# Optimization experiments

Measured on AMD Instinct MI355X. Metric: run time of the kernel, lower is better.

The kernel has to match this reference:

```python
import jax, jax.numpy as jnp
import numpy as np

D_IN = 1024
D_OUT = 1024

def setup_inputs() -> dict:
    key = jax.random.key(0)
    ks = jax.random.split(key, 7)
    s = 1.0 / np.sqrt(D_IN)
    x = jax.random.normal(ks[0], (4, 2048, D_IN), dtype=jnp.float32)
    Wq = jax.random.uniform(ks[1], (D_IN, D_OUT), jnp.float32, -s, s)
    Wk = jax.random.uniform(ks[2], (D_IN, D_OUT), jnp.float32, -s, s)
    Wv = jax.random.uniform(ks[3], (D_IN, D_OUT), jnp.float32, -s, s)
    bq = jax.random.uniform(ks[4], (D_OUT,), jnp.float32, -s, s)
    bk = jax.random.uniform(ks[5], (D_OUT,), jnp.float32, -s, s)
    bv = jax.random.uniform(ks[6], (D_OUT,), jnp.float32, -s, s)
    return {"x": x, "Wq": Wq, "Wk": Wk, "Wv": Wv, "bq": bq, "bk": bk, "bv": bv}

def reference(x, Wq, Wk, Wv, bq, bk, bv):
    # x: [b, n, d_in]
    q = jnp.einsum('bnd,de->bne', x, Wq) + bq
    k = jnp.einsum('bnd,de->bne', x, Wk) + bk
    v = jnp.einsum('bnd,de->bne', x, Wv) + bv
    scale = 1.0 / jnp.sqrt(jnp.asarray(k.shape[-1], dtype=x.dtype))
    scores = jnp.einsum('bqe,bke->bqk', q, k) * scale  # [b, n, n]
    weights = jax.nn.softmax(scores, axis=-1)
    return jnp.einsum('bqk,bke->bqe', weights, v)
```

## Files before the change

kernel.cpp:

```cpp
#include <hip/hip_runtime.h>
#include <cstdint>

typedef __bf16 bf16x8 __attribute__((ext_vector_type(8)));
typedef float f32x16 __attribute__((ext_vector_type(16)));
typedef float f32x4 __attribute__((ext_vector_type(4)));

__device__ __forceinline__ unsigned short f2b(float f) {
    union { float f; uint32_t u; } x; x.f = f;
    uint32_t r = (x.u + 0x7fffu + ((x.u >> 16) & 1u)) >> 16;
    return (unsigned short)r;
}
__device__ __forceinline__ float b2f(unsigned short h) {
    union { float f; uint32_t u; } x; x.u = ((uint32_t)h) << 16;
    return x.f;
}

__global__ __launch_bounds__(256) void convert_x_kernel(const float* __restrict__ x,
                                                        unsigned short* __restrict__ xb) {
    int i = (blockIdx.x * 256 + threadIdx.x) * 4;
    float4 v = *(const float4*)(x + i);
    ushort4 o;
    o.x = f2b(v.x); o.y = f2b(v.y); o.z = f2b(v.z); o.w = f2b(v.w);
    *(ushort4*)(xb + i) = o;
}

__global__ __launch_bounds__(1024) void transpose_w_kernel(const float* __restrict__ Wq,
                                                           const float* __restrict__ Wk,
                                                           const float* __restrict__ Wv,
                                                           unsigned short* __restrict__ Wt) {
    __shared__ float tile[32][33];
    const float* W = (blockIdx.z == 0) ? Wq : (blockIdx.z == 1) ? Wk : Wv;
    int n0 = blockIdx.x * 32, k0 = blockIdx.y * 32;
    int tx = threadIdx.x, ty = threadIdx.y;
    tile[ty][tx] = W[(k0 + ty) * 1024 + n0 + tx];
    __syncthreads();
    Wt[((long)blockIdx.z * 1024 + n0 + ty) * 1024 + k0 + tx] = f2b(tile[tx][ty]);
}

template <int EPI>
__global__ __launch_bounds__(256) void gemm32(const unsigned short* __restrict__ A, int lda, long sA,
                                              const unsigned short* __restrict__ Bm, int ldb, long sB,
                                              void* __restrict__ Cv, long sC, int K,
                                              const float* __restrict__ bq, const float* __restrict__ bk,
                                              const float* __restrict__ bv,
                                              unsigned short* __restrict__ Qb,
                                              unsigned short* __restrict__ Kb,
                                              unsigned short* __restrict__ Vt) {
    __shared__ unsigned short As0[128 * 64];
    __shared__ unsigned short Bs0[128 * 64];
    __shared__ unsigned short As1[128 * 64];
    __shared__ unsigned short Bs1[128 * 64];

    const int tid = threadIdx.x;
    const int wave = tid >> 6, lane = tid & 63;
    const int h = lane >> 5;
    const int l31 = lane & 31;
    const int wm = wave >> 1, wn = wave & 1;
    const long bm = (long)blockIdx.y * 128;
    const long bn = (long)blockIdx.x * 128;

    const unsigned short* Ab = A + (long)blockIdx.z * sA;
    const unsigned short* Bb = Bm + (long)blockIdx.z * sB;

    f32x16 acc[2][2];
#pragma unroll
    for (int mi = 0; mi < 2; ++mi) {
#pragma unroll
        for (int ni = 0; ni < 2; ++ni) {
#pragma unroll
            for (int r = 0; r < 16; ++r) acc[mi][ni][r] = 0.0f;
        }
    }

    const int srow_in = lane >> 3;
    const int cswz = (lane & 7) ^ srow_in;
    const unsigned short* aptr[4];
    const unsigned short* bptr[4];
    int sloff[4];
#pragma unroll
    for (int j = 0; j < 4; ++j) {
        const int row = j * 32 + wave * 8 + srow_in;
        aptr[j] = Ab + (bm + row) * (long)lda + cswz * 8;
        bptr[j] = Bb + (bn + row) * (long)ldb + cswz * 8;
        sloff[j] = (j * 32 + wave * 8) * 64;
    }

    const int arow0 = (wm * 64 + l31) * 64;
    const int brow0 = (wn * 64 + l31) * 64;
    int sw[4];
#pragma unroll
    for (int kh = 0; kh < 4; ++kh)
        sw[kh] = (((2 * kh + h) ^ (lane & 7)) * 8);

#define STAGE(AsB, BsB, kofs)                                                                           \
    do {                                                                                                \
        _Pragma("unroll")                                                                               \
        for (int j = 0; j < 4; ++j) {                                                                   \
            __builtin_amdgcn_global_load_lds(                                                           \
                (const __attribute__((address_space(1))) void*)(aptr[j] + (kofs)),                      \
                (__attribute__((address_space(3))) void*)(&AsB[sloff[j]]), 16, 0, 0);                   \
            __builtin_amdgcn_global_load_lds(                                                           \
                (const __attribute__((address_space(1))) void*)(bptr[j] + (kofs)),                      \
                (__attribute__((address_space(3))) void*)(&BsB[sloff[j]]), 16, 0, 0);                   \
        }                                                                                               \
    } while (0)

#define COMPUTE_T(AsB, BsB)                                                                             \
    do {                                                                                                \
        _Pragma("unroll")                                                                               \
        for (int kp = 0; kp < 2; ++kp) {                                                                \
            bf16x8 af[2][2], bfr[2][2];                                                                 \
            _Pragma("unroll")                                                                           \
            for (int mi = 0; mi < 2; ++mi) {                                                            \
                _Pragma("unroll")                                                                       \
                for (int kk = 0; kk < 2; ++kk) {                                                        \
                    af[mi][kk] = *(const bf16x8*)&AsB[arow0 + mi * 32 * 64 + sw[kp * 2 + kk]];          \
                }                                                                                       \
            }                                                                                           \
            _Pragma("unroll")                                                                           \
            for (int ni = 0; ni < 2; ++ni) {                                                            \
                _Pragma("unroll")                                                                       \
                for (int kk = 0; kk < 2; ++kk) {                                                        \
                    bfr[ni][kk] = *(const bf16x8*)&BsB[brow0 + ni * 32 * 64 + sw[kp * 2 + kk]];         \
                }                                                                                       \
            }                                                                                           \
            _Pragma("unroll")                                                                           \
            for (int kk = 0; kk < 2; ++kk) {                                                            \
                _Pragma("unroll")                                                                       \
                for (int mi = 0; mi < 2; ++mi) {                                                        \
                    _Pragma("unroll")                                                                   \
                    for (int ni = 0; ni < 2; ++ni) {                                                    \
                        acc[mi][ni] = __builtin_amdgcn_mfma_f32_32x32x16_bf16(af[mi][kk], bfr[ni][kk],  \
                                                                              acc[mi][ni], 0, 0, 0);    \
                    }                                                                                   \
                }                                                                                       \
            }                                                                                           \
        }                                                                                               \
    } while (0)

    STAGE(As0, Bs0, 0);

    for (int k0 = 0; k0 < K; k0 += 128) {
        __syncthreads();
        STAGE(As1, Bs1, k0 + 64);
        COMPUTE_T(As0, Bs0);
        __syncthreads();
        if (k0 + 128 < K) STAGE(As0, Bs0, k0 + 128);
        COMPUTE_T(As1, Bs1);
    }

#undef STAGE
#undef COMPUTE_T

#pragma unroll
    for (int mi = 0; mi < 2; ++mi) {
#pragma unroll
        for (int ni = 0; ni < 2; ++ni) {
            const f32x16 a = acc[mi][ni];
            const long col = bn + wn * 64 + ni * 32 + l31;
            const long rowB = bm + wm * 64 + mi * 32 + h * 4;
            if constexpr (EPI == 0) {
                if (col < 1024) {
                    const float bias = bq[col];
#pragma unroll
                    for (int g = 0; g < 4; ++g) {
#pragma unroll
                        for (int r = 0; r < 4; ++r)
                            Qb[(rowB + g * 8 + r) * 1024 + col] = f2b((a[g * 4 + r] + bias) * 0.03125f);
                    }
                } else if (col < 2048) {
                    const float bias = bk[col - 1024];
#pragma unroll
                    for (int g = 0; g < 4; ++g) {
#pragma unroll
                        for (int r = 0; r < 4; ++r)
                            Kb[(rowB + g * 8 + r) * 1024 + (col - 1024)] = f2b(a[g * 4 + r] + bias);
                    }
                } else {
                    const float bias = bv[col - 2048];
#pragma unroll
                    for (int g = 0; g < 4; ++g) {
                        const long row0 = rowB + g * 8;
                        const long batch = row0 >> 11;
                        const int n = (int)(row0 & 2047);
                        ushort4 o;
                        o.x = f2b(a[g * 4 + 0] + bias);
                        o.y = f2b(a[g * 4 + 1] + bias);
                        o.z = f2b(a[g * 4 + 2] + bias);
                        o.w = f2b(a[g * 4 + 3] + bias);
                        *(ushort4*)&Vt[(batch * 1024 + (col - 2048)) * 2048 + n] = o;
                    }
                }
            } else if constexpr (EPI == 1) {
                unsigned short* S = (unsigned short*)Cv + (long)blockIdx.z * sC;
#pragma unroll
                for (int g = 0; g < 4; ++g) {
#pragma unroll
                    for (int r = 0; r < 4; ++r)
                        S[(rowB + g * 8 + r) * 2048 + col] = f2b(a[g * 4 + r]);
                }
            } else {
                float* O = (float*)Cv + (long)blockIdx.z * sC;
#pragma unroll
                for (int g = 0; g < 4; ++g) {
#pragma unroll
                    for (int r = 0; r < 4; ++r)
                        O[(rowB + g * 8 + r) * 1024 + col] = a[g * 4 + r];
                }
            }
        }
    }
}

template <int EPI>
__global__ __launch_bounds__(512, 2) void gemm256(const unsigned short* __restrict__ A, int lda, long sA,
                                                  const unsigned short* __restrict__ Bm, int ldb, long sB,
                                                  void* __restrict__ Cv, long sC, int K,
                                                  const float* __restrict__ bq, const float* __restrict__ bk,
                                                  const float* __restrict__ bv,
                                                  unsigned short* __restrict__ Qb,
                                                  unsigned short* __restrict__ Kb,
                                                  unsigned short* __restrict__ Vt) {
    __shared__ __align__(16) unsigned short Ah0_0[128 * 64];
    __shared__ __align__(16) unsigned short Ah1_0[128 * 64];
    __shared__ __align__(16) unsigned short Bh0_0[128 * 64];
    __shared__ __align__(16) unsigned short Bh1_0[128 * 64];
    __shared__ __align__(16) unsigned short Ah0_1[128 * 64];
    __shared__ __align__(16) unsigned short Ah1_1[128 * 64];
    __shared__ __align__(16) unsigned short Bh0_1[128 * 64];
    __shared__ __align__(16) unsigned short Bh1_1[128 * 64];

    const int tid = threadIdx.x;
    const int w = tid >> 6, l = tid & 63;
    const int wm = w >> 2, wn = w & 3;
    const long bm = (long)blockIdx.y * 256;
    const long bn = (long)blockIdx.x * 256;
    const unsigned short* Ab = A + (long)blockIdx.z * sA;
    const unsigned short* Bb = Bm + (long)blockIdx.z * sB;

    const int lrow = l >> 3;
    const int lchunk = (l & 7) ^ lrow;
    const int fr = l & 15, fg = l >> 4;
    const int kofs0 = ((fg) ^ (l & 7)) * 8;
    const int kofs1 = ((4 + fg) ^ (l & 7)) * 8;
    const int abase = (wm * 64 + fr) * 64;
    const int bbase = (wn * 32 + fr) * 64;

    f32x4 acc[8][4];
#pragma unroll
    for (int mi = 0; mi < 8; ++mi) {
#pragma unroll
        for (int ni = 0; ni < 4; ++ni) {
#pragma unroll
            for (int r = 0; r < 4; ++r) acc[mi][ni][r] = 0.0f;
        }
    }

#define ISSUE_A(DST, hh, T)                                                                              \
    {                                                                                                    \
        const int kk_ = ((T) * 64 < K) ? (T) * 64 : (K - 64);                                            \
        _Pragma("unroll")                                                                                \
        for (int j = 0; j < 2; ++j) {                                                                    \
            const int grow = (hh) * 64 + j * 128 + w * 8;                                                \
            const int arow = j * 64 + w * 8;                                                             \
            __builtin_amdgcn_global_load_lds(                                                            \
                (const __attribute__((address_space(1))) void*)(Ab + (bm + grow + lrow) * (long)lda + kk_ + lchunk * 8), \
                (__attribute__((address_space(3))) void*)(&DST[arow * 64]), 16, 0, 0);                   \
        }                                                                                                \
    }
#define ISSUE_B(DST, hh, T)                                                                              \
    {                                                                                                    \
        const int kk_ = ((T) * 64 < K) ? (T) * 64 : (K - 64);                                            \
        _Pragma("unroll")                                                                                \
        for (int j = 0; j < 2; ++j) {                                                                    \
            const int gb = (hh) * 32 + (w >> 2) * 64 + (w & 3) * 8 + j * 128;                            \
            const int brow_ = (j * 2 + (w >> 2)) * 32 + (w & 3) * 8;                                     \
            __builtin_amdgcn_global_load_lds(                                                            \
                (const __attribute__((address_space(1))) void*)(Bb + (bn + gb + lrow) * (long)ldb + kk_ + lchunk * 8), \
                (__attribute__((address_space(3))) void*)(&DST[brow_ * 64]), 16, 0, 0);                  \
        }                                                                                                \
    }
#define WAITV(n) asm volatile("s_waitcnt vmcnt(" #n ")" ::: "memory")

#define PHASE256(AARR, BARR, QM, QN, ISSUE_STMT, WAIT_STMT)                                              \
    {                                                                                                    \
        bf16x8 a_[4][2], b_[2][2];                                                                       \
        _Pragma("unroll")                                                                                \
        for (int mi = 0; mi < 4; ++mi) {                                                                 \
            a_[mi][0] = *(const bf16x8*)&AARR[abase + mi * 1024 + kofs0];                                \
            a_[mi][1] = *(const bf16x8*)&AARR[abase + mi * 1024 + kofs1];                                \
        }                                                                                                \
        _Pragma("unroll")                                                                                \
        for (int ni = 0; ni < 2; ++ni) {                                                                 \
            b_[ni][0] = *(const bf16x8*)&BARR[bbase + ni * 1024 + kofs0];                                \
            b_[ni][1] = *(const bf16x8*)&BARR[bbase + ni * 1024 + kofs1];                                \
        }                                                                                                \
        ISSUE_STMT;                                                                                      \
        __builtin_amdgcn_s_barrier();                                                                    \
        __builtin_amdgcn_sched_barrier(0);                                                               \
        __builtin_amdgcn_s_setprio(1);                                                                   \
        _Pragma("unroll")                                                                                \
        for (int ks = 0; ks < 2; ++ks) {                                                                 \
            _Pragma("unroll")                                                                            \
            for (int mi = 0; mi < 4; ++mi) {                                                             \
                _Pragma("unroll")                                                                        \
                for (int ni = 0; ni < 2; ++ni) {                                                         \
                    acc[(QM)*4 + mi][(QN)*2 + ni] = __builtin_amdgcn_mfma_f32_16x16x32_bf16(             \
                        a_[mi][ks], b_[ni][ks], acc[(QM)*4 + mi][(QN)*2 + ni], 0, 0, 0);                 \
                }                                                                                        \
            }                                                                                            \
        }                                                                                                \
        __builtin_amdgcn_s_setprio(0);                                                                   \
        WAIT_STMT;                                                                                       \
        __builtin_amdgcn_s_barrier();                                                                    \
        __builtin_amdgcn_sched_barrier(0);                                                               \
    }

    ISSUE_A(Ah0_0, 0, 0);
    ISSUE_B(Bh0_0, 0, 0);
    ISSUE_A(Ah1_0, 1, 0);
    ISSUE_B(Bh1_0, 1, 0);
    ISSUE_A(Ah0_1, 0, 1);
    ISSUE_B(Bh0_1, 0, 1);
    WAITV(4);
    __builtin_amdgcn_s_barrier();
    __builtin_amdgcn_sched_barrier(0);

    const int NT = K >> 6;
    for (int it = 0; it < NT; it += 2) {
        PHASE256(Ah0_0, Bh0_0, 0, 0, ISSUE_A(Ah1_1, 1, it + 1), WAITV(6));
        PHASE256(Ah0_0, Bh1_0, 0, 1, ISSUE_B(Bh1_1, 1, it + 1), ((void)0));
        PHASE256(Ah1_0, Bh0_0, 1, 0, ISSUE_A(Ah0_0, 0, it + 2), ((void)0));
        PHASE256(Ah1_0, Bh1_0, 1, 1, ISSUE_B(Bh0_0, 0, it + 2), WAITV(8));
        PHASE256(Ah0_1, Bh0_1, 0, 0, ISSUE_A(Ah1_0, 1, it + 2), WAITV(6));
        PHASE256(Ah0_1, Bh1_1, 0, 1, ISSUE_B(Bh1_0, 1, it + 2), ((void)0));
        PHASE256(Ah1_1, Bh0_1, 1, 0, ISSUE_A(Ah0_1, 0, it + 3), ((void)0));
        PHASE256(Ah1_1, Bh1_1, 1, 1, ISSUE_B(Bh0_1, 0, it + 3), WAITV(8));
    }

    asm volatile("s_waitcnt vmcnt(0)" ::: "memory");

#undef ISSUE_A
#undef ISSUE_B
#undef WAITV
#undef PHASE256

#pragma unroll
    for (int mi = 0; mi < 8; ++mi) {
        const long grow = bm + wm * 128 + mi * 16 + fg * 4;
#pragma unroll
        for (int ni = 0; ni < 4; ++ni) {
            const long gcol = bn + wn * 64 + ni * 16 + fr;
            const f32x4 a = acc[mi][ni];
            if constexpr (EPI == 0) {
                if (gcol < 1024) {
                    const float bias = bq[gcol];
#pragma unroll
                    for (int r = 0; r < 4; ++r)
                        Qb[(grow + r) * 1024 + gcol] = f2b((a[r] + bias) * 0.03125f);
                } else if (gcol < 2048) {
                    const float bias = bk[gcol - 1024];
#pragma unroll
                    for (int r = 0; r < 4; ++r)
                        Kb[(grow + r) * 1024 + (gcol - 1024)] = f2b(a[r] + bias);
                } else {
                    const float bias = bv[gcol - 2048];
                    const long batch = grow >> 11;
                    const int n = (int)(grow & 2047);
                    ushort4 o;
                    o.x = f2b(a[0] + bias);
                    o.y = f2b(a[1] + bias);
                    o.z = f2b(a[2] + bias);
                    o.w = f2b(a[3] + bias);
                    *(ushort4*)&Vt[(batch * 1024 + (gcol - 2048)) * 2048 + n] = o;
                }
            } else {
                unsigned short* S = (unsigned short*)Cv + (long)blockIdx.z * sC;
#pragma unroll
                for (int r = 0; r < 4; ++r)
                    S[(grow + r) * 2048 + gcol] = f2b(a[r]);
            }
        }
    }
}

__global__ __launch_bounds__(256) void softmax_kernel(unsigned short* __restrict__ S) {
    const long row = blockIdx.x;
    unsigned short* p = S + row * 2048;
    const int tid = threadIdx.x;
    const int wave = tid >> 6, lane = tid & 63;

    ushort4 u0 = *(const ushort4*)&p[tid * 8];
    ushort4 u1 = *(const ushort4*)&p[tid * 8 + 4];
    float v[8];
    v[0] = b2f(u0.x); v[1] = b2f(u0.y); v[2] = b2f(u0.z); v[3] = b2f(u0.w);
    v[4] = b2f(u1.x); v[5] = b2f(u1.y); v[6] = b2f(u1.z); v[7] = b2f(u1.w);

    float m = v[0];
#pragma unroll
    for (int j = 1; j < 8; ++j) m = fmaxf(m, v[j]);
#pragma unroll
    for (int off = 32; off; off >>= 1) m = fmaxf(m, __shfl_xor(m, off, 64));
    __shared__ float redm[4];
    __shared__ float reds[4];
    if (lane == 0) redm[wave] = m;
    __syncthreads();
    m = fmaxf(fmaxf(redm[0], redm[1]), fmaxf(redm[2], redm[3]));

    float s = 0.0f;
#pragma unroll
    for (int j = 0; j < 8; ++j) { v[j] = __expf(v[j] - m); s += v[j]; }
#pragma unroll
    for (int off = 32; off; off >>= 1) s += __shfl_xor(s, off, 64);
    if (lane == 0) reds[wave] = s;
    __syncthreads();
    s = reds[0] + reds[1] + reds[2] + reds[3];
    const float inv = 1.0f / s;

    u0.x = f2b(v[0] * inv); u0.y = f2b(v[1] * inv); u0.z = f2b(v[2] * inv); u0.w = f2b(v[3] * inv);
    u1.x = f2b(v[4] * inv); u1.y = f2b(v[5] * inv); u1.z = f2b(v[6] * inv); u1.w = f2b(v[7] * inv);
    *(ushort4*)&p[tid * 8] = u0;
    *(ushort4*)&p[tid * 8 + 4] = u1;
}

extern "C" void kernel_launch(void* const* d_in, const int* in_sizes, int n_in,
                              void* d_out, int out_size, void* d_ws, size_t ws_size,
                              hipStream_t stream) {
    const float* x  = (const float*)d_in[0];
    const float* Wq = (const float*)d_in[1];
    const float* Wk = (const float*)d_in[2];
    const float* Wv = (const float*)d_in[3];
    const float* bq = (const float*)d_in[4];
    const float* bk = (const float*)d_in[5];
    const float* bv = (const float*)d_in[6];
    float* out = (float*)d_out;

    char* ws = (char*)d_ws;
    unsigned short* xb = (unsigned short*)ws; ws += 8192L * 1024 * 2;
    unsigned short* Wt = (unsigned short*)ws; ws += 3072L * 1024 * 2;
    unsigned short* Qb = (unsigned short*)ws; ws += 8192L * 1024 * 2;
    unsigned short* Kb = (unsigned short*)ws; ws += 8192L * 1024 * 2;
    unsigned short* Vt = (unsigned short*)ws; ws += 4L * 1024 * 2048 * 2;
    unsigned short* S  = (unsigned short*)ws; ws += 4L * 2048 * 2048 * 2;

    convert_x_kernel<<<8192, 256, 0, stream>>>(x, xb);
    transpose_w_kernel<<<dim3(32, 32, 3), dim3(32, 32), 0, stream>>>(Wq, Wk, Wv, Wt);
    gemm256<0><<<dim3(12, 32, 1), 512, 0, stream>>>(xb, 1024, 0, Wt, 1024, 0,
                                                    nullptr, 0, 1024, bq, bk, bv, Qb, Kb, Vt);
    gemm256<1><<<dim3(8, 8, 4), 512, 0, stream>>>(Qb, 1024, 2048L * 1024, Kb, 1024, 2048L * 1024,
                                                  S, 2048L * 2048, 1024,
                                                  nullptr, nullptr, nullptr, nullptr, nullptr, nullptr);
    softmax_kernel<<<8192, 256, 0, stream>>>(S);
    gemm32<2><<<dim3(8, 16, 4), 256, 0, stream>>>(S, 2048, 2048L * 2048, Vt, 2048, 2048L * 1024,
                                                  out, 2048L * 1024, 2048,
                                                  nullptr, nullptr, nullptr, nullptr, nullptr, nullptr);
}
```

Measured before the change: 296.8 us.

## Reorder GEMM quadrant phases to reuse A/B register fragments across MFMA blocks

Reworks the 256x256 GEMM main loop so each k-tile runs four MFMA quadrants in the order (0,0),(0,1),(1,1),(1,0). This lets fragments already in registers be reused, cutting LDS reads from A+B per phase to one half-tile per phase. The prologue now prefetches a full extra k-tile (both halves), and global-to-LDS refills are reissued at new points with adjusted vmcnt waits. The cost is more live VGPRs for fragments and a changed prefetch/wait schedule that needs the LDS buffer reuse ordering to stay correct.

```diff
diff --git a/kernel.cpp b/kernel.cpp
--- a/kernel.cpp
+++ b/kernel.cpp
@@ -256,6 +256,10 @@
         }
     }
 
+    bf16x8 af[4][2];
+    bf16x8 b0_[2][2];
+    bf16x8 b1_[2][2];
+
 #define ISSUE_A(DST, hh, T)                                                                              \
     {                                                                                                    \
         const int kk_ = ((T) * 64 < K) ? (T) * 64 : (K - 64);                                            \
@@ -282,38 +286,63 @@
     }
 #define WAITV(n) asm volatile("s_waitcnt vmcnt(" #n ")" ::: "memory")
 
-#define PHASE256(AARR, BARR, QM, QN, ISSUE_STMT, WAIT_STMT)                                              \
-    {                                                                                                    \
-        bf16x8 a_[4][2], b_[2][2];                                                                       \
+#define READ_A(SRC)                                                                                      \
+    _Pragma("unroll")                                                                                    \
+    for (int mi = 0; mi < 4; ++mi) {                                                                     \
+        af[mi][0] = *(const bf16x8*)&SRC[abase + mi * 1024 + kofs0];                                     \
+        af[mi][1] = *(const bf16x8*)&SRC[abase + mi * 1024 + kofs1];                                     \
+    }
+#define READ_B(DSTV, SRC)                                                                                \
+    _Pragma("unroll")                                                                                    \
+    for (int ni = 0; ni < 2; ++ni) {                                                                     \
+        DSTV[ni][0] = *(const bf16x8*)&SRC[bbase + ni * 1024 + kofs0];                                   \
+        DSTV[ni][1] = *(const bf16x8*)&SRC[bbase + ni * 1024 + kofs1];                                   \
+    }
+#define MFMA8(QM, QN, BF)                                                                                \
+    __builtin_amdgcn_s_setprio(1);                                                                       \
+    _Pragma("unroll")                                                                                    \
+    for (int ks = 0; ks < 2; ++ks) {                                                                     \
         _Pragma("unroll")                                                                                \
         for (int mi = 0; mi < 4; ++mi) {                                                                 \
-            a_[mi][0] = *(const bf16x8*)&AARR[abase + mi * 1024 + kofs0];                                \
-            a_[mi][1] = *(const bf16x8*)&AARR[abase + mi * 1024 + kofs1];                                \
-        }                                                                                                \
-        _Pragma("unroll")                                                                                \
-        for (int ni = 0; ni < 2; ++ni) {                                                                 \
-            b_[ni][0] = *(const bf16x8*)&BARR[bbase + ni * 1024 + kofs0];                                \
-            b_[ni][1] = *(const bf16x8*)&BARR[bbase + ni * 1024 + kofs1];                                \
-        }                                                                                                \
-        ISSUE_STMT;                                                                                      \
-        __builtin_amdgcn_s_barrier();                                                                    \
-        __builtin_amdgcn_sched_barrier(0);                                                               \
-        __builtin_amdgcn_s_setprio(1);                                                                   \
-        _Pragma("unroll")                                                                                \
-        for (int ks = 0; ks < 2; ++ks) {                                                                 \
             _Pragma("unroll")                                                                            \
-            for (int mi = 0; mi < 4; ++mi) {                                                             \
-                _Pragma("unroll")                                                                        \
-                for (int ni = 0; ni < 2; ++ni) {                                                         \
-                    acc[(QM)*4 + mi][(QN)*2 + ni] = __builtin_amdgcn_mfma_f32_16x16x32_bf16(             \
-                        a_[mi][ks], b_[ni][ks], acc[(QM)*4 + mi][(QN)*2 + ni], 0, 0, 0);                 \
-                }                                                                                        \
+            for (int ni = 0; ni < 2; ++ni) {                                                             \
+                acc[(QM)*4 + mi][(QN)*2 + ni] = __builtin_amdgcn_mfma_f32_16x16x32_bf16(                 \
+                    af[mi][ks], BF[ni][ks], acc[(QM)*4 + mi][(QN)*2 + ni], 0, 0, 0);                     \
             }                                                                                            \
         }                                                                                                \
-        __builtin_amdgcn_s_setprio(0);                                                                   \
-        WAIT_STMT;                                                                                       \
-        __builtin_amdgcn_s_barrier();                                                                    \
-        __builtin_amdgcn_sched_barrier(0);                                                               \
+    }                                                                                                    \
+    __builtin_amdgcn_s_setprio(0);
+
+#define BAR() __builtin_amdgcn_s_barrier()
+#define SCHED0() __builtin_amdgcn_sched_barrier(0)
+
+#define TILE256(AH0, AH1, BH0, BH1, U)                                                                   \
+    {                                                                                                    \
+                                                     \
+        READ_A(AH0);                                                                                     \
+        READ_B(b0_, BH0);                                                                                \
+        BAR();                                                                                           \
+        MFMA8(0, 0, b0_);                                                                                \
+        BAR(); SCHED0();                                                                                 \
+                                     \
+        READ_B(b1_, BH1);                                                                                \
+        ISSUE_A(AH0, 0, (U) + 2);                                                                        \
+        ISSUE_B(BH0, 0, (U) + 2);                                                                        \
+        BAR();                                                                                           \
+        MFMA8(0, 1, b1_);                                                                                \
+        BAR(); SCHED0();                                                                                 \
+                                                        \
+        READ_A(AH1);                                                                                     \
+        ISSUE_B(BH1, 1, (U) + 2);                                                                        \
+        BAR();                                                                                           \
+        MFMA8(1, 1, b1_);                                                                                \
+        BAR(); SCHED0();                                                                                 \
+                        \
+        ISSUE_A(AH1, 1, (U) + 2);                                                                        \
+        BAR();                                                                                           \
+        MFMA8(1, 0, b0_);                                                                                \
+        WAITV(8);                                                                                        \
+        BAR(); SCHED0();                                                                                 \
     }
 
     ISSUE_A(Ah0_0, 0, 0);
@@ -322,20 +351,15 @@
     ISSUE_B(Bh1_0, 1, 0);
     ISSUE_A(Ah0_1, 0, 1);
     ISSUE_B(Bh0_1, 0, 1);
-    WAITV(4);
-    __builtin_amdgcn_s_barrier();
-    __builtin_amdgcn_sched_barrier(0);
+    ISSUE_A(Ah1_1, 1, 1);
+    ISSUE_B(Bh1_1, 1, 1);
+    WAITV(8);
+    BAR(); SCHED0();
 
     const int NT = K >> 6;
-    for (int it = 0; it < NT; it += 2) {
-        PHASE256(Ah0_0, Bh0_0, 0, 0, ISSUE_A(Ah1_1, 1, it + 1), WAITV(6));
-        PHASE256(Ah0_0, Bh1_0, 0, 1, ISSUE_B(Bh1_1, 1, it + 1), ((void)0));
-        PHASE256(Ah1_0, Bh0_0, 1, 0, ISSUE_A(Ah0_0, 0, it + 2), ((void)0));
-        PHASE256(Ah1_0, Bh1_0, 1, 1, ISSUE_B(Bh0_0, 0, it + 2), WAITV(8));
-        PHASE256(Ah0_1, Bh0_1, 0, 0, ISSUE_A(Ah1_0, 1, it + 2), WAITV(6));
-        PHASE256(Ah0_1, Bh1_1, 0, 1, ISSUE_B(Bh1_0, 1, it + 2), ((void)0));
-        PHASE256(Ah1_1, Bh0_1, 1, 0, ISSUE_A(Ah0_1, 0, it + 3), ((void)0));
-        PHASE256(Ah1_1, Bh1_1, 1, 1, ISSUE_B(Bh0_1, 0, it + 3), WAITV(8));
+    for (int u = 0; u < NT; u += 2) {
+        TILE256(Ah0_0, Ah1_0, Bh0_0, Bh1_0, u);
+        TILE256(Ah0_1, Ah1_1, Bh0_1, Bh1_1, u + 1);
     }
 
     asm volatile("s_waitcnt vmcnt(0)" ::: "memory");
@@ -343,7 +367,12 @@
 #undef ISSUE_A
 #undef ISSUE_B
 #undef WAITV
-#undef PHASE256
+#undef READ_A
+#undef READ_B
+#undef MFMA8
+#undef BAR
+#undef SCHED0
+#undef TILE256
 
 #pragma unroll
     for (int mi = 0; mi < 8; ++mi) {
```

Measured after the change: 275.5 us. 7.2% less time.
